# Performance work log

Hardware: AMD Instinct MI355X
Metric: run time of the kernel (lower is better)

The kernel has to match this reference:

```python
import jax, jax.numpy as jnp
import numpy as np

HEADS = 16
DIM_HEAD = 64
NEG_INF = -1e30


def _rope_cos_sin(seq_len, dim_head, dtype):
    inv_freq = 1.0 / (10000.0 ** (jnp.arange(0, dim_head, 2, dtype=jnp.float32) / dim_head))
    t = jnp.arange(seq_len, dtype=jnp.float32)
    freqs = jnp.einsum('i,j->ij', t, inv_freq)          # [n, dh/2]
    emb = jnp.concatenate([freqs, freqs], axis=-1)       # [n, dh]
    return jnp.cos(emb).astype(dtype), jnp.sin(emb).astype(dtype)


def _rotate_half(x):
    x1, x2 = jnp.split(x, 2, axis=-1)
    return jnp.concatenate([-x2, x1], axis=-1)


def setup_inputs() -> dict:
    key = jax.random.key(0)
    k1, k2, k3 = jax.random.split(key, 3)
    dim = HEADS * DIM_HEAD  # 1024
    x = jax.random.normal(k1, (2, 2048, dim), dtype=jnp.float32)
    w_qkv = jax.random.normal(k2, (dim, 3 * dim), dtype=jnp.float32) * (dim ** -0.5)
    w_out = jax.random.normal(k3, (dim, dim), dtype=jnp.float32) * (dim ** -0.5)
    return {"x": x, "w_qkv": w_qkv, "w_out": w_out}


def reference(x, w_qkv, w_out):
    b, n, d = x.shape
    h, dh = HEADS, DIM_HEAD
    scale = dh ** -0.5

    qkv = x @ w_qkv                                      # [b, n, 3*h*dh]
    q, k, v = jnp.split(qkv, 3, axis=-1)
    reshape = lambda t: t.reshape(b, n, h, dh).transpose(0, 2, 1, 3)  # b h n dh
    q, k, v = reshape(q), reshape(k), reshape(v)

    cos, sin = _rope_cos_sin(n, dh, x.dtype)
    cos = cos[None, None, :, :]
    sin = sin[None, None, :, :]
    q = q * cos + _rotate_half(q) * sin
    k = k * cos + _rotate_half(k) * sin

    scores = jnp.einsum('bhid,bhjd->bhij', q, k) * scale  # [b, h, n, n]
    causal = jnp.triu(jnp.ones((n, n), dtype=bool), k=1)
    scores = jnp.where(causal[None, None, :, :], NEG_INF, scores)
    attn = jax.nn.softmax(scores, axis=-1)

    out = jnp.einsum('bhij,bhjd->bhid', attn, v)          # [b, h, n, dh]
    out = out.transpose(0, 2, 1, 3).reshape(b, n, h * dh)
    return out @ w_out
```

## Files before the change

### kernel.cpp

```cpp
#include <hip/hip_runtime.h>

#define SEQ 2048
#define NH 16
#define DH 64
#define DMODEL 1024
#define NQKV 3072

typedef __attribute__((ext_vector_type(8))) short bf16x8;
typedef __attribute__((ext_vector_type(4))) short bf16x4;
typedef __attribute__((ext_vector_type(4))) float f32x4;

#define GLOAD16(src, dst)                                                              \
  __builtin_amdgcn_global_load_lds((const __attribute__((address_space(1))) void*)(src), \
                                   (__attribute__((address_space(3))) void*)(dst), 16, 0, 0)

__device__ __forceinline__ unsigned short f2bf(float f) {
  union { float f; unsigned u; } v; v.f = f;
  unsigned r = v.u + 0x7FFFu + ((v.u >> 16) & 1u);
  return (unsigned short)(r >> 16);
}

__device__ __forceinline__ unsigned pkbf(float a, float b) {
  unsigned r;
  asm("v_cvt_pk_bf16_f32 %0, %1, %2" : "=v"(r) : "v"(a), "v"(b));
  return r;
}

__device__ __forceinline__ void transw_body(const float* __restrict__ in,
                                            unsigned short* __restrict__ out,
                                            int K, int N, int k0, int n0, int tid,
                                            float (*Ts)[65]) {
#pragma unroll
  for (int p = 0; p < 4; ++p) {
    int id = p * 256 + tid;
    int r = id >> 4, c4 = (id & 15) * 4;
    const f32x4 v = *reinterpret_cast<const f32x4*>(&in[(size_t)(k0 + r) * N + n0 + c4]);
    Ts[r][c4] = v[0]; Ts[r][c4 + 1] = v[1]; Ts[r][c4 + 2] = v[2]; Ts[r][c4 + 3] = v[3];
  }
  __syncthreads();
#pragma unroll
  for (int p = 0; p < 2; ++p) {
    int id = p * 256 + tid;
    int n = id >> 3, k8 = (id & 7) * 8;
    unsigned short tmp[8];
#pragma unroll
    for (int i = 0; i < 8; ++i) tmp[i] = f2bf(Ts[k8 + i][n]);
    *reinterpret_cast<bf16x8*>(&out[(size_t)(n0 + n) * K + k0 + k8]) =
        *reinterpret_cast<bf16x8*>(tmp);
  }
}

__global__ __launch_bounds__(256) void prep_kernel(
    const float* __restrict__ x, const float* __restrict__ w_qkv,
    const float* __restrict__ w_out, unsigned short* __restrict__ Xb,
    unsigned short* __restrict__ WqkvT, unsigned short* __restrict__ WoutT,
    float* __restrict__ cost, float* __restrict__ sint) {
  __shared__ float Ts[64][65];
  const int tid = threadIdx.x;
  const int id = blockIdx.x;
  if (id < 2048) {
    int idx = id * 256 + tid;
    const f32x4 v0 = *reinterpret_cast<const f32x4*>(&x[(size_t)idx * 8]);
    const f32x4 v1 = *reinterpret_cast<const f32x4*>(&x[(size_t)idx * 8 + 4]);
    bf16x8 o;
    o[0] = (short)f2bf(v0[0]); o[1] = (short)f2bf(v0[1]);
    o[2] = (short)f2bf(v0[2]); o[3] = (short)f2bf(v0[3]);
    o[4] = (short)f2bf(v1[0]); o[5] = (short)f2bf(v1[1]);
    o[6] = (short)f2bf(v1[2]); o[7] = (short)f2bf(v1[3]);
    *reinterpret_cast<bf16x8*>(&Xb[(size_t)idx * 8]) = o;
  } else if (id < 2816) {
    int t = id - 2048;
    transw_body(w_qkv, WqkvT, DMODEL, NQKV, (t & 15) * 64, (t >> 4) * 64, tid, Ts);
  } else if (id < 3072) {
    int t = id - 2816;
    transw_body(w_out, WoutT, DMODEL, DMODEL, (t & 15) * 64, (t >> 4) * 64, tid, Ts);
  } else {
    int idx = (id - 3072) * 256 + tid;
    int t = idx >> 5, j = idx & 31;
    float inv = powf(10000.0f, -(float)(2 * j) / 64.0f);
    float a = (float)t * inv;
    cost[idx] = cosf(a);
    sint[idx] = sinf(a);
  }
}

__global__ __launch_bounds__(256) void gemm_qkv_kernel(
    const unsigned short* __restrict__ Xb, const unsigned short* __restrict__ BT,
    unsigned short* __restrict__ Qb, unsigned short* __restrict__ Kb,
    unsigned short* __restrict__ Vtg,
    const float* __restrict__ cost, const float* __restrict__ sint) {
  __shared__ unsigned short As[2][8192];
  __shared__ unsigned short Bs[2][8192];

  const int tid = threadIdx.x;
  const int lane = tid & 63;
  const int w = tid >> 6;
  const int lam = lane & 15;
  const int g = lane >> 4;
  const int wr = w >> 1, wc = w & 1;
  const int rowBase = blockIdx.x * 128;
  const int colBase = blockIdx.y * 128;

  f32x4 acc[4][4];
#pragma unroll
  for (int m = 0; m < 4; ++m)
#pragma unroll
    for (int n = 0; n < 4; ++n) acc[m][n] = (f32x4){0.f, 0.f, 0.f, 0.f};

#define GSTAGE(buf, kk0)                                                               \
  {                                                                                    \
    _Pragma("unroll") for (int c = 0; c < 4; ++c) {                                    \
      int ch = c * 256 + w * 64 + lane;                                                \
      int row = ch >> 3, q = ch & 7;                                                   \
      GLOAD16(Xb + (size_t)(rowBase + row) * DMODEL + (kk0) + ((q ^ (row & 7)) * 8),   \
              &As[buf][0] + (c * 256 + w * 64) * 8);                                   \
      GLOAD16(BT + (size_t)(colBase + row) * DMODEL + (kk0) + ((q ^ (row & 7)) * 8),   \
              &Bs[buf][0] + (c * 256 + w * 64) * 8);                                   \
    }                                                                                  \
  }

  GSTAGE(0, 0);

  for (int kb = 0; kb < 16; ++kb) {
    if (kb + 1 < 16) {
      GSTAGE((kb + 1) & 1, (kb + 1) * 64);
      asm volatile("s_waitcnt vmcnt(8)" ::: "memory");
    } else {
      asm volatile("s_waitcnt vmcnt(0)" ::: "memory");
    }
    __builtin_amdgcn_s_barrier();
    const int cb = kb & 1;
#pragma unroll
    for (int kh = 0; kh < 2; ++kh) {
      bf16x8 a[4], b[4];
#pragma unroll
      for (int m = 0; m < 4; ++m) {
        int row = wr * 64 + m * 16 + lam;
        a[m] = *reinterpret_cast<bf16x8*>(&As[cb][row * 64 + (((kh * 4 + g) ^ (row & 7)) * 8)]);
      }
#pragma unroll
      for (int n = 0; n < 4; ++n) {
        int row = wc * 64 + n * 16 + lam;
        b[n] = *reinterpret_cast<bf16x8*>(&Bs[cb][row * 64 + (((kh * 4 + g) ^ (row & 7)) * 8)]);
      }
      __builtin_amdgcn_s_setprio(1);
#pragma unroll
      for (int m = 0; m < 4; ++m)
#pragma unroll
        for (int n = 0; n < 4; ++n)
          acc[m][n] = __builtin_amdgcn_mfma_f32_16x16x32_bf16(a[m], b[n], acc[m][n], 0, 0, 0);
      __builtin_amdgcn_s_setprio(0);
    }
    asm volatile("s_waitcnt lgkmcnt(0)" ::: "memory");
    __builtin_amdgcn_s_barrier();
  }
#undef GSTAGE

  const int mat = blockIdx.y >> 3;
  if (mat < 2) {
    unsigned short* dst = mat ? Kb : Qb;
    const float sc = mat ? 1.0f : 0.125f;
    const int h = ((colBase & 1023) + wc * 64) >> 6;
#pragma unroll
    for (int m = 0; m < 4; ++m) {
#pragma unroll
      for (int r = 0; r < 4; ++r) {
        int row = rowBase + wr * 64 + m * 16 + g * 4 + r;
        int bi = row >> 11, t = row & 2047;
        unsigned short* out = &dst[(size_t)((bi * NH + h) * SEQ + t) * DH];
#pragma unroll
        for (int n = 0; n < 2; ++n) {
          int j = n * 16 + lam;
          float c = cost[t * 32 + j], s = sint[t * 32 + j];
          float x0 = acc[m][n][r], x1 = acc[m][n + 2][r];
          out[j] = f2bf((x0 * c - x1 * s) * sc);
          out[j + 32] = f2bf((x1 * c + x0 * s) * sc);
        }
      }
    }
  } else {
    unsigned short (*Vbuf)[44] = reinterpret_cast<unsigned short(*)[44]>(&As[0][0]);
    const int b = rowBase >> 11, t0 = rowBase & 2047;
#pragma unroll
    for (int cc = 0; cc < 4; ++cc) {
      __syncthreads();
      if (wc == (cc >> 1)) {
        const int n0 = (cc & 1) * 2;
#pragma unroll
        for (int m = 0; m < 4; ++m)
#pragma unroll
          for (int r = 0; r < 4; ++r)
#pragma unroll
            for (int n2 = 0; n2 < 2; ++n2)
              Vbuf[wr * 64 + m * 16 + g * 4 + r][n2 * 16 + lam] = f2bf(acc[m][n0 + n2][r]);
      }
      __syncthreads();
      const int colq0 = colBase - 2048 + cc * 32;
#pragma unroll
      for (int p2 = 0; p2 < 2; ++p2) {
        int ch = p2 * 256 + tid;
        int d = ch & 31, tq = (ch >> 5) * 8;
        unsigned short tmp[8];
#pragma unroll
        for (int i = 0; i < 8; ++i) tmp[i] = Vbuf[tq + i][d];
        int col = colq0 + d;
        int h = col >> 6, dd = col & 63;
        *reinterpret_cast<bf16x8*>(&Vtg[((size_t)(b * NH + h) * DH + dd) * SEQ + t0 + tq]) =
            *reinterpret_cast<bf16x8*>(tmp);
      }
    }
  }
}

__global__ __launch_bounds__(256) void attn_kernel(
    const unsigned short* __restrict__ Qb, const unsigned short* __restrict__ Kb,
    const unsigned short* __restrict__ Vtg, unsigned short* __restrict__ Ob) {
  __shared__ unsigned short Ks[2][8192];
  __shared__ unsigned short Vs[2][8192];
  __shared__ unsigned short Ps[4][2048];

  const int tid = threadIdx.x;
  const int lane = tid & 63;
  const int w = tid >> 6;
  const int lam = lane & 15;
  const int g = lane >> 4;
  const int bh = blockIdx.x;
  const int p = blockIdx.y;
  const int qtA = p, qtB = 31 - p;
  const int nA = (p >> 1) + 1;
  const int nB = ((31 - p) >> 1) + 1;
  const int nT = nA + nB;
  const int ql = w * 16 + lam;

  const unsigned short* kallbase = Kb + (size_t)bh * SEQ * DH;
  const unsigned short* vallbase = Vtg + (size_t)bh * DH * SEQ;

  bf16x8 qb0, qb1;
  f32x4 oacc[4], sa0[4], sa1[4];
  float mr, lr;

#define LOADQ(qt)                                                                     \
  {                                                                                   \
    const unsigned short* qrow = Qb + ((size_t)bh * SEQ + (qt) * 64 + w * 16 + lam) * DH; \
    qb0 = *reinterpret_cast<const bf16x8*>(&qrow[g * 8]);                             \
    qb1 = *reinterpret_cast<const bf16x8*>(&qrow[g * 8 + 32]);                        \
  }
#define RESET_STATE()                                                                 \
  {                                                                                   \
    _Pragma("unroll") for (int f = 0; f < 4; ++f) oacc[f] = (f32x4){0.f, 0.f, 0.f, 0.f}; \
    mr = -1e30f; lr = 0.f;                                                            \
  }
#define STAGE(buf, jt)                                                                \
  {                                                                                   \
    const unsigned short* kb2 = kallbase + (size_t)(jt) * 128 * DH;                   \
    const unsigned short* vb2 = vallbase + (size_t)(jt) * 128;                        \
    _Pragma("unroll") for (int c = 0; c < 4; ++c) {                                   \
      int id = c * 256 + w * 64 + lane;                                               \
      int kr = id >> 3, kq = id & 7;                                                  \
      GLOAD16(kb2 + kr * DH + ((kq ^ (kr & 7)) * 8), &Ks[buf][0] + id * 8);           \
      int vr = id >> 4, vq = id & 15;                                                 \
      GLOAD16(vb2 + (size_t)vr * SEQ + ((vq ^ (vr & 15)) * 8), &Vs[buf][0] + id * 8); \
    }                                                                                 \
  }
#define FLUSHO(qt)                                                                    \
  {                                                                                   \
    const int b = bh >> 4, h = bh & 15;                                               \
    float rinv = 1.0f / lr;                                                           \
    _Pragma("unroll") for (int r = 0; r < 4; ++r) {                                   \
      int n = (qt) * 64 + w * 16 + g * 4 + r;                                         \
      float inv = __shfl(rinv, g * 4 + r);                                            \
      unsigned short* orow = &Ob[(size_t)(b * SEQ + n) * DMODEL + h * DH];            \
      _Pragma("unroll") for (int f = 0; f < 4; ++f) orow[f * 16 + lam] = f2bf(oacc[f][r] * inv); \
    }                                                                                 \
  }

  RESET_STATE();
  LOADQ(qtA);
  STAGE(0, 0);
  asm volatile("s_waitcnt vmcnt(0)" ::: "memory");
  __syncthreads();

  int cur = 0;
  for (int i = 0; i < nT; ++i) {
    const int onA = (i < nA);
    const int qt = onA ? qtA : qtB;
    const int j = onA ? i : (i - nA);

    if (i + 1 < nT) {
      const int jn = (i + 1 < nA) ? (i + 1) : (i + 1 - nA);
      STAGE(cur ^ 1, jn);
    }

    const int t1 = 2 * j + 1;
    const bool diag0 = (2 * j == qt);
    const bool diag1 = (t1 == qt);
    const bool skip1 = (t1 > qt);

#pragma unroll
    for (int f = 0; f < 4; ++f) {
      sa0[f] = (f32x4){0.f, 0.f, 0.f, 0.f};
      sa1[f] = (f32x4){0.f, 0.f, 0.f, 0.f};
    }
    __builtin_amdgcn_s_setprio(1);
#pragma unroll
    for (int f = 0; f < 4; ++f) {
      int kr = f * 16 + lam;
      bf16x8 k0 = *reinterpret_cast<bf16x8*>(&Ks[cur][kr * 64 + ((g ^ (kr & 7)) * 8)]);
      bf16x8 k1 = *reinterpret_cast<bf16x8*>(&Ks[cur][kr * 64 + (((g + 4) ^ (kr & 7)) * 8)]);
      sa0[f] = __builtin_amdgcn_mfma_f32_16x16x32_bf16(k0, qb0, sa0[f], 0, 0, 0);
      sa0[f] = __builtin_amdgcn_mfma_f32_16x16x32_bf16(k1, qb1, sa0[f], 0, 0, 0);
    }
    if (!skip1) {
#pragma unroll
      for (int f = 0; f < 4; ++f) {
        int kr = 64 + f * 16 + lam;
        bf16x8 k0 = *reinterpret_cast<bf16x8*>(&Ks[cur][kr * 64 + ((g ^ (kr & 7)) * 8)]);
        bf16x8 k1 = *reinterpret_cast<bf16x8*>(&Ks[cur][kr * 64 + (((g + 4) ^ (kr & 7)) * 8)]);
        sa1[f] = __builtin_amdgcn_mfma_f32_16x16x32_bf16(k0, qb0, sa1[f], 0, 0, 0);
        sa1[f] = __builtin_amdgcn_mfma_f32_16x16x32_bf16(k1, qb1, sa1[f], 0, 0, 0);
      }
    }
    __builtin_amdgcn_s_setprio(0);

    if (diag0) {
#pragma unroll
      for (int f = 0; f < 4; ++f)
#pragma unroll
        for (int r = 0; r < 4; ++r)
          if (f * 16 + g * 4 + r > ql) sa0[f][r] = -1e30f;
    }
    if (diag1) {
#pragma unroll
      for (int f = 0; f < 4; ++f)
#pragma unroll
        for (int r = 0; r < 4; ++r)
          if (f * 16 + g * 4 + r > ql) sa1[f][r] = -1e30f;
    }

    float mx = -1e30f;
#pragma unroll
    for (int f = 0; f < 4; ++f)
#pragma unroll
      for (int r = 0; r < 4; ++r) mx = fmaxf(mx, sa0[f][r]);
    if (!skip1) {
#pragma unroll
      for (int f = 0; f < 4; ++f)
#pragma unroll
        for (int r = 0; r < 4; ++r) mx = fmaxf(mx, sa1[f][r]);
    }
    mx = fmaxf(mx, __shfl_xor(mx, 16));
    mx = fmaxf(mx, __shfl_xor(mx, 32));
    float mn = fmaxf(mr, mx);
    float alpha = __expf(mr - mn);
    mr = mn;

    float sum = 0.f;
#pragma unroll
    for (int f = 0; f < 4; ++f)
#pragma unroll
      for (int r = 0; r < 4; ++r) {
        sa0[f][r] = __expf(sa0[f][r] - mn);
        sum += sa0[f][r];
      }
    if (!skip1) {
#pragma unroll
      for (int f = 0; f < 4; ++f)
#pragma unroll
        for (int r = 0; r < 4; ++r) {
          sa1[f][r] = __expf(sa1[f][r] - mn);
          sum += sa1[f][r];
        }
    }
    sum += __shfl_xor(sum, 16);
    sum += __shfl_xor(sum, 32);
    lr = lr * alpha + sum;

#pragma unroll
    for (int r = 0; r < 4; ++r) {
      float af = __shfl(alpha, g * 4 + r);
#pragma unroll
      for (int f = 0; f < 4; ++f) oacc[f][r] *= af;
    }

#pragma unroll
    for (int f = 0; f < 4; ++f) {
      uint2 u;
      u.x = pkbf(sa0[f][0], sa0[f][1]);
      u.y = pkbf(sa0[f][2], sa0[f][3]);
      int chunk = f * 2 + (g >> 1);
      *reinterpret_cast<uint2*>(
          &Ps[w][lam * 128 + ((chunk ^ (lam & 15)) * 8) + ((g & 1) * 4)]) = u;
    }
    if (!skip1) {
#pragma unroll
      for (int f = 0; f < 4; ++f) {
        uint2 u;
        u.x = pkbf(sa1[f][0], sa1[f][1]);
        u.y = pkbf(sa1[f][2], sa1[f][3]);
        int chunk = 8 + f * 2 + (g >> 1);
        *reinterpret_cast<uint2*>(
            &Ps[w][lam * 128 + ((chunk ^ (lam & 15)) * 8) + ((g & 1) * 4)]) = u;
      }
    }

    bf16x8 pa0 = *reinterpret_cast<bf16x8*>(&Ps[w][lam * 128 + ((g ^ (lam & 15)) * 8)]);
    bf16x8 pa1 = *reinterpret_cast<bf16x8*>(&Ps[w][lam * 128 + (((4 + g) ^ (lam & 15)) * 8)]);
    __builtin_amdgcn_s_setprio(1);
#pragma unroll
    for (int f = 0; f < 4; ++f) {
      int vr = f * 16 + lam;
      bf16x8 v0 = *reinterpret_cast<bf16x8*>(&Vs[cur][vr * 128 + ((g ^ (vr & 15)) * 8)]);
      bf16x8 v1 = *reinterpret_cast<bf16x8*>(&Vs[cur][vr * 128 + (((4 + g) ^ (vr & 15)) * 8)]);
      oacc[f] = __builtin_amdgcn_mfma_f32_16x16x32_bf16(pa0, v0, oacc[f], 0, 0, 0);
      oacc[f] = __builtin_amdgcn_mfma_f32_16x16x32_bf16(pa1, v1, oacc[f], 0, 0, 0);
    }
    __builtin_amdgcn_s_setprio(0);
    if (!skip1) {
      bf16x8 pa2 = *reinterpret_cast<bf16x8*>(&Ps[w][lam * 128 + (((8 + g) ^ (lam & 15)) * 8)]);
      bf16x8 pa3 = *reinterpret_cast<bf16x8*>(&Ps[w][lam * 128 + (((12 + g) ^ (lam & 15)) * 8)]);
      __builtin_amdgcn_s_setprio(1);
#pragma unroll
      for (int f = 0; f < 4; ++f) {
        int vr = f * 16 + lam;
        bf16x8 v2 = *reinterpret_cast<bf16x8*>(&Vs[cur][vr * 128 + (((8 + g) ^ (vr & 15)) * 8)]);
        bf16x8 v3 = *reinterpret_cast<bf16x8*>(&Vs[cur][vr * 128 + (((12 + g) ^ (vr & 15)) * 8)]);
        oacc[f] = __builtin_amdgcn_mfma_f32_16x16x32_bf16(pa2, v2, oacc[f], 0, 0, 0);
        oacc[f] = __builtin_amdgcn_mfma_f32_16x16x32_bf16(pa3, v3, oacc[f], 0, 0, 0);
      }
      __builtin_amdgcn_s_setprio(0);
    }

    if (i == nA - 1) {
      FLUSHO(qtA);
      RESET_STATE();
      LOADQ(qtB);
    }

    asm volatile("s_waitcnt vmcnt(0)" ::: "memory");
    __syncthreads();
    cur ^= 1;
  }
  FLUSHO(qtB);
#undef LOADQ
#undef RESET_STATE
#undef STAGE
#undef FLUSHO
}

__global__ __launch_bounds__(256) void gemm_out_kernel(
    const unsigned short* __restrict__ A, const unsigned short* __restrict__ BT,
    float* __restrict__ C) {
  __shared__ unsigned short As[2][8192];
  __shared__ unsigned short Bs[2][8192];

  const int tid = threadIdx.x;
  const int lane = tid & 63;
  const int w = tid >> 6;
  const int lam = lane & 15;
  const int g = lane >> 4;
  const int wr = w >> 1, wc = w & 1;
  const int rowBase = blockIdx.x * 128;
  const int colBase = blockIdx.y * 128;

  f32x4 acc[4][4];
#pragma unroll
  for (int m = 0; m < 4; ++m)
#pragma unroll
    for (int n = 0; n < 4; ++n) acc[m][n] = (f32x4){0.f, 0.f, 0.f, 0.f};

#define GSTAGE(buf, kk0)                                                               \
  {                                                                                    \
    _Pragma("unroll") for (int c = 0; c < 4; ++c) {                                    \
      int ch = c * 256 + w * 64 + lane;                                                \
      int row = ch >> 3, q = ch & 7;                                                   \
      GLOAD16(A + (size_t)(rowBase + row) * DMODEL + (kk0) + ((q ^ (row & 7)) * 8),    \
              &As[buf][0] + (c * 256 + w * 64) * 8);                                   \
      GLOAD16(BT + (size_t)(colBase + row) * DMODEL + (kk0) + ((q ^ (row & 7)) * 8),   \
              &Bs[buf][0] + (c * 256 + w * 64) * 8);                                   \
    }                                                                                  \
  }

  GSTAGE(0, 0);

  for (int kb = 0; kb < 16; ++kb) {
    if (kb + 1 < 16) {
      GSTAGE((kb + 1) & 1, (kb + 1) * 64);
      asm volatile("s_waitcnt vmcnt(8)" ::: "memory");
    } else {
      asm volatile("s_waitcnt vmcnt(0)" ::: "memory");
    }
    __builtin_amdgcn_s_barrier();
    const int cb = kb & 1;
#pragma unroll
    for (int kh = 0; kh < 2; ++kh) {
      bf16x8 a[4], b[4];
#pragma unroll
      for (int m = 0; m < 4; ++m) {
        int row = wr * 64 + m * 16 + lam;
        a[m] = *reinterpret_cast<bf16x8*>(&As[cb][row * 64 + (((kh * 4 + g) ^ (row & 7)) * 8)]);
      }
#pragma unroll
      for (int n = 0; n < 4; ++n) {
        int row = wc * 64 + n * 16 + lam;
        b[n] = *reinterpret_cast<bf16x8*>(&Bs[cb][row * 64 + (((kh * 4 + g) ^ (row & 7)) * 8)]);
      }
      __builtin_amdgcn_s_setprio(1);
#pragma unroll
      for (int m = 0; m < 4; ++m)
#pragma unroll
        for (int n = 0; n < 4; ++n)
          acc[m][n] = __builtin_amdgcn_mfma_f32_16x16x32_bf16(a[m], b[n], acc[m][n], 0, 0, 0);
      __builtin_amdgcn_s_setprio(0);
    }
    asm volatile("s_waitcnt lgkmcnt(0)" ::: "memory");
    __builtin_amdgcn_s_barrier();
  }
#undef GSTAGE

#pragma unroll
  for (int m = 0; m < 4; ++m)
#pragma unroll
    for (int r = 0; r < 4; ++r) {
      int row = rowBase + wr * 64 + m * 16 + g * 4 + r;
#pragma unroll
      for (int n = 0; n < 4; ++n)
        C[(size_t)row * DMODEL + colBase + wc * 64 + n * 16 + lam] = acc[m][n][r];
    }
}

extern "C" void kernel_launch(void* const* d_in, const int* in_sizes, int n_in,
                              void* d_out, int out_size, void* d_ws, size_t ws_size,
                              hipStream_t stream) {
  const float* x = (const float*)d_in[0];
  const float* w_qkv = (const float*)d_in[1];
  const float* w_out = (const float*)d_in[2];
  float* out = (float*)d_out;

  char* ws = (char*)d_ws;
  const size_t MB = 1024 * 1024;
  unsigned short* WqkvT = (unsigned short*)(ws);
  float* cost = (float*)(ws + 6 * MB);
  float* sint = cost + SEQ * 32;
  unsigned short* Ob = (unsigned short*)(ws);
  unsigned short* WoutT = (unsigned short*)(ws + 8 * MB);
  unsigned short* Qb = (unsigned short*)(ws + 10 * MB);
  unsigned short* Kb = (unsigned short*)(ws + 18 * MB);
  unsigned short* Vtg = (unsigned short*)(ws + 26 * MB);
  unsigned short* Xb = (unsigned short*)d_out;

  prep_kernel<<<3328, 256, 0, stream>>>(x, w_qkv, w_out, Xb, WqkvT, WoutT, cost, sint);
  gemm_qkv_kernel<<<dim3(32, 24), 256, 0, stream>>>(Xb, WqkvT, Qb, Kb, Vtg, cost, sint);
  attn_kernel<<<dim3(32, 16), 256, 0, stream>>>(Qb, Kb, Vtg, Ob);
  gemm_out_kernel<<<dim3(32, 8), 256, 0, stream>>>(Ob, WoutT, out);
}
```

Baseline: 118.0 us.

## Enlarge QKV GEMM tile to 256x256 with 8 waves and interleaved staging

The QKV projection GEMM moves from 128x128 tiles with 4 waves to 256x256 tiles with 8 waves (512 threads). Global-to-LDS staging for the next K tile is split into quarter chunks placed between barrier-separated MFMA groups, in a ping-pong schedule. The goal is more operand reuse per byte loaded and better overlap of memory traffic with MFMA work. In exchange the grid shrinks from 768 to 192 blocks, so fewer blocks than CUs and lower occupancy. It also uses more LDS and registers and adds many barriers, and the V transpose epilogue becomes more serialized.

```diff
diff --git a/kernel.cpp b/kernel.cpp
--- a/kernel.cpp
+++ b/kernel.cpp
@@ -84,88 +84,118 @@
   }
 }
 
-__global__ __launch_bounds__(256) void gemm_qkv_kernel(
+__global__ __launch_bounds__(512) void gemm_qkv_kernel(
     const unsigned short* __restrict__ Xb, const unsigned short* __restrict__ BT,
     unsigned short* __restrict__ Qb, unsigned short* __restrict__ Kb,
     unsigned short* __restrict__ Vtg,
     const float* __restrict__ cost, const float* __restrict__ sint) {
-  __shared__ unsigned short As[2][8192];
-  __shared__ unsigned short Bs[2][8192];
+  __shared__ unsigned short As[2][16384];
+  __shared__ unsigned short Bs[2][16384];
 
   const int tid = threadIdx.x;
   const int lane = tid & 63;
   const int w = tid >> 6;
   const int lam = lane & 15;
   const int g = lane >> 4;
-  const int wr = w >> 1, wc = w & 1;
-  const int rowBase = blockIdx.x * 128;
-  const int colBase = blockIdx.y * 128;
-
-  f32x4 acc[4][4];
-#pragma unroll
-  for (int m = 0; m < 4; ++m)
+  const int wr = w >> 2;
+  const int wc = w & 3;
+  const int rowBase = blockIdx.x * 256;
+  const int colBase = blockIdx.y * 256;
+
+  f32x4 acc[8][4];
+#pragma unroll
+  for (int m = 0; m < 8; ++m)
 #pragma unroll
     for (int n = 0; n < 4; ++n) acc[m][n] = (f32x4){0.f, 0.f, 0.f, 0.f};
 
-#define GSTAGE(buf, kk0)                                                               \
+  bf16x8 pa[4][2];
+  bf16x8 pb[4][2];
+
+#define STAGEH(OPBASE, LDS, buf, half, kt)                                             \
   {                                                                                    \
-    _Pragma("unroll") for (int c = 0; c < 4; ++c) {                                    \
-      int ch = c * 256 + w * 64 + lane;                                                \
-      int row = ch >> 3, q = ch & 7;                                                   \
-      GLOAD16(Xb + (size_t)(rowBase + row) * DMODEL + (kk0) + ((q ^ (row & 7)) * 8),   \
-              &As[buf][0] + (c * 256 + w * 64) * 8);                                   \
-      GLOAD16(BT + (size_t)(colBase + row) * DMODEL + (kk0) + ((q ^ (row & 7)) * 8),   \
-              &Bs[buf][0] + (c * 256 + w * 64) * 8);                                   \
+    _Pragma("unroll") for (int c = 0; c < 2; ++c) {                                    \
+      int id = c * 512 + tid;                                                          \
+      int r128 = id >> 3, q = id & 7;                                                  \
+      GLOAD16(OPBASE + (size_t)((half) * 128 + r128) * DMODEL + (kt) * 64 +            \
+                  ((q ^ (r128 & 7)) * 8),                                              \
+              &LDS[buf][0] + (half) * 8192 + (c * 512 + w * 64) * 8);                  \
     }                                                                                  \
   }
 
-  GSTAGE(0, 0);
-
-  for (int kb = 0; kb < 16; ++kb) {
-    if (kb + 1 < 16) {
-      GSTAGE((kb + 1) & 1, (kb + 1) * 64);
-      asm volatile("s_waitcnt vmcnt(8)" ::: "memory");
-    } else {
-      asm volatile("s_waitcnt vmcnt(0)" ::: "memory");
-    }
+  const unsigned short* Abase = Xb + (size_t)rowBase * DMODEL;
+  const unsigned short* Bbase = BT + (size_t)colBase * DMODEL;
+
+#define RD_A(buf, mg)                                                                  \
+  _Pragma("unroll") for (int mi = 0; mi < 4; ++mi) {                                   \
+    int row = wr * 128 + (mg) * 64 + mi * 16 + lam;                                    \
+    _Pragma("unroll") for (int ks = 0; ks < 2; ++ks)                                   \
+      pa[mi][ks] = *reinterpret_cast<bf16x8*>(                                         \
+          &As[buf][row * 64 + (((ks * 4 + g) ^ (row & 7)) * 8)]);                      \
+  }
+#define RD_B(buf, nlo)                                                                 \
+  _Pragma("unroll") for (int ni = 0; ni < 2; ++ni) {                                   \
+    int row = wc * 64 + ((nlo) + ni) * 16 + lam;                                       \
+    _Pragma("unroll") for (int ks = 0; ks < 2; ++ks)                                   \
+      pb[(nlo) + ni][ks] = *reinterpret_cast<bf16x8*>(                                 \
+          &Bs[buf][row * 64 + (((ks * 4 + g) ^ (row & 7)) * 8)]);                      \
+  }
+#define MFMA8(mg, nlo)                                                                 \
+  __builtin_amdgcn_s_setprio(1);                                                       \
+  _Pragma("unroll") for (int mi = 0; mi < 4; ++mi)                                     \
+    _Pragma("unroll") for (int ni = 0; ni < 2; ++ni)                                   \
+      _Pragma("unroll") for (int ks = 0; ks < 2; ++ks)                                 \
+        acc[(mg) * 4 + mi][(nlo) + ni] = __builtin_amdgcn_mfma_f32_16x16x32_bf16(      \
+            pa[mi][ks], pb[(nlo) + ni][ks], acc[(mg) * 4 + mi][(nlo) + ni], 0, 0, 0);  \
+  __builtin_amdgcn_s_setprio(0);
+#define BAR() __builtin_amdgcn_s_barrier();
+
+#define KTILE(buf, sbuf, skt, DOSTAGE)                                                 \
+  {                                                                                    \
+    RD_A(buf, 0) RD_B(buf, 0)                                                          \
+    if (DOSTAGE) STAGEH(Abase, As, sbuf, 0, skt);                                      \
+    BAR() MFMA8(0, 0) BAR()                                                            \
+    RD_B(buf, 2)                                                                       \
+    if (DOSTAGE) STAGEH(Abase, As, sbuf, 1, skt);                                      \
+    BAR() MFMA8(0, 2) BAR()                                                            \
+    RD_A(buf, 1)                                                                       \
+    if (DOSTAGE) STAGEH(Bbase, Bs, sbuf, 0, skt);                                      \
+    BAR() MFMA8(1, 2) BAR()                                                            \
+    if (DOSTAGE) STAGEH(Bbase, Bs, sbuf, 1, skt);                                      \
+    BAR() MFMA8(1, 0) BAR()                                                            \
+  }
+
+  STAGEH(Abase, As, 0, 0, 0);
+  STAGEH(Abase, As, 0, 1, 0);
+  STAGEH(Bbase, Bs, 0, 0, 0);
+  STAGEH(Bbase, Bs, 0, 1, 0);
+  asm volatile("s_waitcnt vmcnt(0)" ::: "memory");
+  __builtin_amdgcn_s_barrier();
+
+  for (int t = 0; t < 8; ++t) {
+    KTILE(0, 1, 2 * t + 1, true);
+    asm volatile("s_waitcnt vmcnt(0)" ::: "memory");
     __builtin_amdgcn_s_barrier();
-    const int cb = kb & 1;
-#pragma unroll
-    for (int kh = 0; kh < 2; ++kh) {
-      bf16x8 a[4], b[4];
-#pragma unroll
-      for (int m = 0; m < 4; ++m) {
-        int row = wr * 64 + m * 16 + lam;
-        a[m] = *reinterpret_cast<bf16x8*>(&As[cb][row * 64 + (((kh * 4 + g) ^ (row & 7)) * 8)]);
-      }
-#pragma unroll
-      for (int n = 0; n < 4; ++n) {
-        int row = wc * 64 + n * 16 + lam;
-        b[n] = *reinterpret_cast<bf16x8*>(&Bs[cb][row * 64 + (((kh * 4 + g) ^ (row & 7)) * 8)]);
-      }
-      __builtin_amdgcn_s_setprio(1);
-#pragma unroll
-      for (int m = 0; m < 4; ++m)
-#pragma unroll
-        for (int n = 0; n < 4; ++n)
-          acc[m][n] = __builtin_amdgcn_mfma_f32_16x16x32_bf16(a[m], b[n], acc[m][n], 0, 0, 0);
-      __builtin_amdgcn_s_setprio(0);
-    }
-    asm volatile("s_waitcnt lgkmcnt(0)" ::: "memory");
+    KTILE(1, 0, 2 * t + 2, (t < 7));
+    asm volatile("s_waitcnt vmcnt(0)" ::: "memory");
     __builtin_amdgcn_s_barrier();
   }
-#undef GSTAGE
-
-  const int mat = blockIdx.y >> 3;
+#undef KTILE
+#undef BAR
+#undef MFMA8
+#undef RD_B
+#undef RD_A
+#undef STAGEH
+
+  const int mat = colBase >> 10;
   if (mat < 2) {
     unsigned short* dst = mat ? Kb : Qb;
     const float sc = mat ? 1.0f : 0.125f;
     const int h = ((colBase & 1023) + wc * 64) >> 6;
 #pragma unroll
-    for (int m = 0; m < 4; ++m) {
+    for (int m = 0; m < 8; ++m) {
 #pragma unroll
       for (int r = 0; r < 4; ++r) {
-        int row = rowBase + wr * 64 + m * 16 + g * 4 + r;
+        int row = rowBase + wr * 128 + m * 16 + g * 4 + r;
         int bi = row >> 11, t = row & 2047;
         unsigned short* out = &dst[(size_t)((bi * NH + h) * SEQ + t) * DH];
 #pragma unroll
@@ -179,33 +209,30 @@
       }
     }
   } else {
-    unsigned short (*Vbuf)[44] = reinterpret_cast<unsigned short(*)[44]>(&As[0][0]);
+    unsigned short (*Vbuf)[40] = reinterpret_cast<unsigned short(*)[40]>(&As[0][0]);
     const int b = rowBase >> 11, t0 = rowBase & 2047;
-#pragma unroll
-    for (int cc = 0; cc < 4; ++cc) {
-      __syncthreads();
-      if (wc == (cc >> 1)) {
-        const int n0 = (cc & 1) * 2;
-#pragma unroll
-        for (int m = 0; m < 4; ++m)
-#pragma unroll
-          for (int r = 0; r < 4; ++r)
-#pragma unroll
-            for (int n2 = 0; n2 < 2; ++n2)
-              Vbuf[wr * 64 + m * 16 + g * 4 + r][n2 * 16 + lam] = f2bf(acc[m][n0 + n2][r]);
-      }
-      __syncthreads();
-      const int colq0 = colBase - 2048 + cc * 32;
-#pragma unroll
-      for (int p2 = 0; p2 < 2; ++p2) {
-        int ch = p2 * 256 + tid;
-        int d = ch & 31, tq = (ch >> 5) * 8;
+    for (int rh = 0; rh < 2; ++rh) {
+      for (int cc = 0; cc < 8; ++cc) {
+        __syncthreads();
+        if (wr == rh && wc == (cc >> 1)) {
+          const int n0 = (cc & 1) * 2;
+#pragma unroll
+          for (int m = 0; m < 8; ++m)
+#pragma unroll
+            for (int r = 0; r < 4; ++r)
+#pragma unroll
+              for (int n2 = 0; n2 < 2; ++n2)
+                Vbuf[m * 16 + g * 4 + r][n2 * 16 + lam] = f2bf(acc[m][n0 + n2][r]);
+        }
+        __syncthreads();
+        int d = tid & 31, tq = (tid >> 5) * 8;
         unsigned short tmp[8];
 #pragma unroll
         for (int i = 0; i < 8; ++i) tmp[i] = Vbuf[tq + i][d];
-        int col = colq0 + d;
+        int col = (colBase - 2048) + cc * 32 + d;
         int h = col >> 6, dd = col & 63;
-        *reinterpret_cast<bf16x8*>(&Vtg[((size_t)(b * NH + h) * DH + dd) * SEQ + t0 + tq]) =
+        *reinterpret_cast<bf16x8*>(
+            &Vtg[((size_t)(b * NH + h) * DH + dd) * SEQ + t0 + rh * 128 + tq]) =
             *reinterpret_cast<bf16x8*>(tmp);
       }
     }
@@ -549,7 +576,7 @@
   unsigned short* Xb = (unsigned short*)d_out;
 
   prep_kernel<<<3328, 256, 0, stream>>>(x, w_qkv, w_out, Xb, WqkvT, WoutT, cost, sint);
-  gemm_qkv_kernel<<<dim3(32, 24), 256, 0, stream>>>(Xb, WqkvT, Qb, Kb, Vtg, cost, sint);
+  gemm_qkv_kernel<<<dim3(16, 12), 512, 0, stream>>>(Xb, WqkvT, Qb, Kb, Vtg, cost, sint);
   attn_kernel<<<dim3(32, 16), 256, 0, stream>>>(Qb, Kb, Vtg, Ob);
   gemm_out_kernel<<<dim3(32, 8), 256, 0, stream>>>(Ob, WoutT, out);
 }
```

Result: slower. 154.3 us (+30.7%).
